# Optimization experiments

Hardware: AMD Instinct MI355X
Metric: run time of the kernel (lower is better)

Reference implementation:

```python
import jax, jax.numpy as jnp
import numpy as np

TEMPERATURE = 0.7
REDUCTION = "mean"
MARGIN = 0.5  # the '+0.5' shift inside exp in the original


def setup_inputs() -> dict:
    key = jax.random.key(0)
    k1, k2 = jax.random.split(key)
    projection = jax.random.normal(k1, (8192, 256), dtype=jnp.float32)
    y = jax.random.randint(k2, (8192,), 0, 10, dtype=jnp.int64)
    return {"projection": projection, "y": y}


def reference(projection, y):
    # L2-normalize rows, cosine similarity matrix [n, n]
    n = projection.shape[0]
    proj = projection / jnp.linalg.norm(projection, axis=1, keepdims=True)
    sim = proj @ proj.T

    eq = (y[:, None] == y[None, :]).astype(sim.dtype)
    same = eq - jnp.eye(n, dtype=sim.dtype)   # same class, excluding self
    diff = 1.0 - eq                            # different class

    # Original per-row loop computes log(1 + sum_{j in diff, k in same}
    #   exp((sim[i,j] - sim[i,k] + 0.5)/t)) which separates as
    #   exp(0.5/t) * (sum_j exp(sim[i,j]/t)) * (sum_k exp(-sim[i,k]/t)).
    # Empty set -> the loop substitutes [0], i.e. that factor becomes exp(0)=1.
    A = jnp.sum(diff * jnp.exp(sim / TEMPERATURE), axis=1)
    B = jnp.sum(same * jnp.exp(-sim / TEMPERATURE), axis=1)
    A = jnp.where(jnp.sum(diff, axis=1) > 0, A, 1.0)
    B = jnp.where(jnp.sum(same, axis=1) > 0, B, 1.0)

    loss_per_row = jnp.log1p(jnp.exp(MARGIN / TEMPERATURE) * A * B)
    if REDUCTION == "mean":
        return jnp.mean(loss_per_row)
    return jnp.sum(loss_per_row)
```

## Files before the change

### kernel.cpp

```cpp
#include <hip/hip_runtime.h>
#include <hip/hip_bf16.h>


#define NF 256
#define TINV (1.0f / 0.7f)
#define SC2 2.0609929398439434f

typedef __attribute__((ext_vector_type(8))) short short8;
typedef __attribute__((ext_vector_type(4))) float float4v;

typedef const __attribute__((address_space(1))) unsigned int glb_u32;
typedef __attribute__((address_space(3))) unsigned int lds_u32;

__global__ __launch_bounds__(256)
void k_prep(const float* __restrict__ P, unsigned short* __restrict__ Pn,
            float* __restrict__ AB) {
    int wave = threadIdx.x >> 6, lane = threadIdx.x & 63;
    int row = blockIdx.x * 4 + wave;
    if (threadIdx.x < 8) AB[blockIdx.x * 8 + threadIdx.x] = 0.f;
    float4 v = *(const float4*)(P + (size_t)row * NF + lane * 4);
    float sq = v.x * v.x + v.y * v.y + v.z * v.z + v.w * v.w;
#pragma unroll
    for (int off = 32; off; off >>= 1) sq += __shfl_xor(sq, off, 64);
    float r = rsqrtf(sq);
    __hip_bfloat16 h0 = __float2bfloat16(v.x * r), h1 = __float2bfloat16(v.y * r),
                   h2 = __float2bfloat16(v.z * r), h3 = __float2bfloat16(v.w * r);
    ushort4 o = { *(unsigned short*)&h0, *(unsigned short*)&h1,
                  *(unsigned short*)&h2, *(unsigned short*)&h3 };
    *(ushort4*)(Pn + (size_t)row * NF + lane * 4) = o;
}

__global__ __launch_bounds__(256, 2)
void k_main(const unsigned short* __restrict__ Pn, const int* __restrict__ y,
            float* __restrict__ Aacc, float* __restrict__ Bacc,
            float* __restrict__ colPart) {
    __shared__ __align__(16) unsigned short Bs[64 * NF];
    __shared__ int yc[256];
    __shared__ float colA[1024], colB[1024];

    const int tid = threadIdx.x;
    int bid = blockIdx.x;
    int C = (int)((sqrtf(4.0f * (float)bid + 1.0f) - 1.0f) * 0.5f);
    while (C * (C + 1) > bid) --C;
    while ((C + 1) * (C + 2) <= bid) ++C;
    const int I = bid - C * (C + 1);
    const int rb = I * 128, cb0 = C * 256;
    const bool colacc = (C > (I >> 1));

    const int lane = tid & 63, wave = tid >> 6;
    const int quad = lane >> 4, l15 = lane & 15;

#define DMA_CHUNK(c)                                                          \
    {                                                                         \
        _Pragma("unroll")                                                     \
        for (int i = 0; i < 8; ++i) {                                         \
            const int kc = wave * 8 + i;                                      \
            const unsigned short* src =                                       \
                Pn + (size_t)(cb0 + (c) * 64 + lane) * NF + kc * 8;           \
            __builtin_amdgcn_global_load_lds((glb_u32*)src,                   \
                (lds_u32*)&Bs[kc * 512], 16, 0, 0);                           \
        }                                                                     \
    }

    DMA_CHUNK(0)

    yc[tid] = y[cb0 + tid];
#pragma unroll
    for (int w = 0; w < 4; ++w) {
        colA[w * 256 + tid] = 0.f;
        colB[w * 256 + tid] = 0.f;
    }

    const unsigned short* pa = Pn + (size_t)(rb + wave * 32 + l15) * NF + quad * 8;
    short8 afr[2][8];
#pragma unroll
    for (int tr = 0; tr < 2; ++tr)
#pragma unroll
        for (int ks = 0; ks < 8; ++ks)
            afr[tr][ks] = *(const short8*)(pa + (size_t)tr * 16 * NF + ks * 32);

    unsigned yis[2];
#pragma unroll
    for (int tr = 0; tr < 2; ++tr) {
        int4 v = *(const int4*)(y + rb + wave * 32 + tr * 16 + quad * 4);
        yis[tr] = (unsigned)(v.x & 255) | ((unsigned)(v.y & 255) << 8) |
                  ((unsigned)(v.z & 255) << 16) | ((unsigned)(v.w & 255) << 24);
    }

    float rA[2][4], rB[2][4];
#pragma unroll
    for (int tr = 0; tr < 2; ++tr)
#pragma unroll
        for (int r = 0; r < 4; ++r) { rA[tr][r] = 0.f; rB[tr][r] = 0.f; }

#pragma unroll 1
    for (int c = 0; c < 4; ++c) {
        __syncthreads();

        float4v acc[2][4];
#pragma unroll
        for (int a = 0; a < 2; ++a)
#pragma unroll
            for (int b = 0; b < 4; ++b) acc[a][b] = (float4v){0.f, 0.f, 0.f, 0.f};

#pragma unroll
        for (int ks = 0; ks < 8; ++ks) {
            short8 fb[4];
#pragma unroll
            for (int tc = 0; tc < 4; ++tc)
                fb[tc] = *(const short8*)&Bs[(ks * 4 + quad) * 512 + (tc * 16 + l15) * 8];
#pragma unroll
            for (int tr = 0; tr < 2; ++tr)
#pragma unroll
                for (int tc = 0; tc < 4; ++tc)
                    acc[tr][tc] = __builtin_amdgcn_mfma_f32_16x16x32_bf16(
                        afr[tr][ks], fb[tc], acc[tr][tc], 0, 0, 0);
        }
        __syncthreads();
        if (c < 3) DMA_CHUNK(c + 1)

#pragma unroll
        for (int tc = 0; tc < 4; ++tc) {
            const int jl = c * 64 + tc * 16 + l15;
            const int yj = yc[jl];
            const int gj = cb0 + jl;
#pragma unroll
            for (int tr = 0; tr < 2; ++tr) {
                const int gi0 = rb + wave * 32 + tr * 16 + quad * 4;
#pragma unroll
                for (int r = 0; r < 4; ++r) {
                    const float s = acc[tr][tc][r];
                    const int cls = (yis[tr] >> (8 * r)) & 255;
                    const bool same = (cls == yj);
                    const float e = exp2f(s * (same ? -SC2 : SC2));
                    rA[tr][r] += same ? 0.f : e;
                    rB[tr][r] += (same && (gi0 + r != gj)) ? e : 0.f;
                }
            }
        }

        if (colacc) {
#pragma unroll
            for (int tc = 0; tc < 4; ++tc) {
                const int jl = c * 64 + tc * 16 + l15;
                const int yj = yc[jl];
                float ca = 0.f, cb = 0.f;
#pragma unroll
                for (int tr = 0; tr < 2; ++tr)
#pragma unroll
                    for (int r = 0; r < 4; ++r) {
                        const float s = acc[tr][tc][r];
                        const int cls = (yis[tr] >> (8 * r)) & 255;
                        const bool same = (cls == yj);
                        const float e = exp2f(s * (same ? -SC2 : SC2));
                        ca += same ? 0.f : e;
                        cb += same ? e : 0.f;
                    }
                ca += __shfl_xor(ca, 16, 64); ca += __shfl_xor(ca, 32, 64);
                cb += __shfl_xor(cb, 16, 64); cb += __shfl_xor(cb, 32, 64);
                if (quad == 0) {
                    colA[wave * 256 + jl] += ca;
                    colB[wave * 256 + jl] += cb;
                }
            }
        }
    }

#pragma unroll
    for (int tr = 0; tr < 2; ++tr)
#pragma unroll
        for (int r = 0; r < 4; ++r) {
#pragma unroll
            for (int off = 1; off < 16; off <<= 1) {
                rA[tr][r] += __shfl_xor(rA[tr][r], off, 64);
                rB[tr][r] += __shfl_xor(rB[tr][r], off, 64);
            }
        }
    if (l15 == 0) {
#pragma unroll
        for (int tr = 0; tr < 2; ++tr)
#pragma unroll
            for (int r = 0; r < 4; ++r) {
                const int gi = rb + wave * 32 + tr * 16 + quad * 4 + r;
                atomicAdd(&Aacc[gi], rA[tr][r]);
                atomicAdd(&Bacc[gi], rB[tr][r]);
            }
    }

    if (colacc) {
        __syncthreads();
        float* cp = colPart + (size_t)bid * 512;
        cp[tid]       = colA[tid] + colA[256 + tid] + colA[512 + tid] + colA[768 + tid];
        cp[256 + tid] = colB[tid] + colB[256 + tid] + colB[512 + tid] + colB[768 + tid];
    }
}

__global__ __launch_bounds__(256)
void k_reduce(const float* __restrict__ colPart, float* __restrict__ Aacc,
              float* __restrict__ Bacc) {
    const int t = threadIdx.x;
    const int jloc = t >> 1, half = t & 1;
    const int j = blockIdx.x * 128 + jloc;
    const int C = j >> 8, o = j & 255;
    const float* p = colPart + (size_t)(C * (C + 1) + half) * 512 + o;
    float sA = 0.f, sB = 0.f;
    for (int I = half; I < 2 * C; I += 2) {
        sA += p[0];
        sB += p[256];
        p += 1024;
    }
    sA += __shfl_xor(sA, 1, 64);
    sB += __shfl_xor(sB, 1, 64);
    if (half == 0) {
        Aacc[j] += sA;
        Bacc[j] += sB;
    }
}

__global__ __launch_bounds__(1024)
void k_final(const float* __restrict__ Aacc, const float* __restrict__ Bacc,
             const int* __restrict__ y, float* __restrict__ out, int n) {
    __shared__ int hist[16];
    __shared__ float red[16];
    const int tid = threadIdx.x;
    if (tid < 16) hist[tid] = 0;
    __syncthreads();
    int loc[10];
#pragma unroll
    for (int cc = 0; cc < 10; ++cc) loc[cc] = 0;
    for (int i = tid; i < n; i += 1024) {
        const int yv = y[i];
#pragma unroll
        for (int cc = 0; cc < 10; ++cc) {
            unsigned long long m = __ballot(yv == cc);
            if ((tid & 63) == 0) loc[cc] += __popcll(m);
        }
    }
    if ((tid & 63) == 0)
#pragma unroll
        for (int cc = 0; cc < 10; ++cc) atomicAdd(&hist[cc], loc[cc]);
    __syncthreads();
    const float M = __expf(0.5f * TINV);
    float s = 0.f;
    for (int i = tid; i < n; i += 1024) {
        const int cc = hist[y[i] & 15];
        const float a = (n - cc) > 0 ? Aacc[i] : 1.0f;
        const float b = (cc - 1) > 0 ? Bacc[i] : 1.0f;
        s += log1pf(M * a * b);
    }
#pragma unroll
    for (int off = 32; off; off >>= 1) s += __shfl_xor(s, off, 64);
    if ((tid & 63) == 0) red[tid >> 6] = s;
    __syncthreads();
    if (tid == 0) {
        float t = 0.f;
#pragma unroll
        for (int w = 0; w < 16; ++w) t += red[w];
        out[0] = t / (float)n;
    }
}

extern "C" void kernel_launch(void* const* d_in, const int* in_sizes, int n_in,
                              void* d_out, int out_size, void* d_ws, size_t ws_size,
                              hipStream_t stream) {
    const float* P = (const float*)d_in[0];
    const int* y   = (const int*)d_in[1];
    float* out     = (float*)d_out;
    const int n = in_sizes[1];

    unsigned short* Pn = (unsigned short*)d_ws;
    float* Aacc = (float*)((char*)d_ws + (size_t)n * NF * 2);
    float* Bacc = Aacc + n;
    float* colPart = Bacc + n;

    const int ng = n / 256;
    k_prep<<<n / 4, 256, 0, stream>>>(P, Pn, Aacc);
    k_main<<<ng * (ng + 1), 256, 0, stream>>>(Pn, y, Aacc, Bacc, colPart);
    k_reduce<<<n / 128, 256, 0, stream>>>(colPart, Aacc, Bacc);
    k_final<<<1, 1024, 0, stream>>>(Aacc, Bacc, y, out, n);
}
```

Measured before the change: 141.6 us.

## Use 128x128 triangular tiles, skip duplicate exps, fuse reduce and final kernels

The main kernel moves from 128x256 column-block tiles to 128x128 tiles over the upper triangle. Off-diagonal tiles now compute each exp once and feed both the row and column accumulators, where before the row pass and the column pass each evaluated the exp separately. Per-wave column buffers in LDS become a shared 128-entry buffer updated with LDS atomics, which shrinks LDS use. The column reduction and final log1p/mean kernels are merged into one multi-block tail kernel that writes the output with a global atomic, removing a launch and the single-block final pass, at the cost of more, smaller main blocks and LDS atomic contention.

After: 141.6 us. Within noise of the previous version (-0.0%).

```diff
diff --git a/kernel.cpp b/kernel.cpp
--- a/kernel.cpp
+++ b/kernel.cpp
@@ -14,10 +14,11 @@
 
 __global__ __launch_bounds__(256)
 void k_prep(const float* __restrict__ P, unsigned short* __restrict__ Pn,
-            float* __restrict__ AB) {
+            float* __restrict__ AB, float* __restrict__ out) {
     int wave = threadIdx.x >> 6, lane = threadIdx.x & 63;
     int row = blockIdx.x * 4 + wave;
     if (threadIdx.x < 8) AB[blockIdx.x * 8 + threadIdx.x] = 0.f;
+    if (blockIdx.x == 0 && threadIdx.x == 0) out[0] = 0.f;
     float4 v = *(const float4*)(P + (size_t)row * NF + lane * 4);
     float sq = v.x * v.x + v.y * v.y + v.z * v.z + v.w * v.w;
 #pragma unroll
@@ -35,17 +36,17 @@
             float* __restrict__ Aacc, float* __restrict__ Bacc,
             float* __restrict__ colPart) {
     __shared__ __align__(16) unsigned short Bs[64 * NF];
-    __shared__ int yc[256];
-    __shared__ float colA[1024], colB[1024];
+    __shared__ int yc[128];
+    __shared__ float colA[128], colB[128];
 
     const int tid = threadIdx.x;
     int bid = blockIdx.x;
-    int C = (int)((sqrtf(4.0f * (float)bid + 1.0f) - 1.0f) * 0.5f);
-    while (C * (C + 1) > bid) --C;
-    while ((C + 1) * (C + 2) <= bid) ++C;
-    const int I = bid - C * (C + 1);
-    const int rb = I * 128, cb0 = C * 256;
-    const bool colacc = (C > (I >> 1));
+    int C2 = (int)((sqrtf(8.0f * (float)bid + 1.0f) - 1.0f) * 0.5f);
+    while ((C2 * (C2 + 1)) / 2 > bid) --C2;
+    while (((C2 + 1) * (C2 + 2)) / 2 <= bid) ++C2;
+    const int I = bid - (C2 * (C2 + 1)) / 2;
+    const int rb = I * 128, cb0 = C2 * 128;
+    const bool offdiag = (I < C2);
 
     const int lane = tid & 63, wave = tid >> 6;
     const int quad = lane >> 4, l15 = lane & 15;
@@ -64,11 +65,10 @@
 
     DMA_CHUNK(0)
 
-    yc[tid] = y[cb0 + tid];
-#pragma unroll
-    for (int w = 0; w < 4; ++w) {
-        colA[w * 256 + tid] = 0.f;
-        colB[w * 256 + tid] = 0.f;
+    if (tid < 128) {
+        yc[tid] = y[cb0 + tid];
+        colA[tid] = 0.f;
+        colB[tid] = 0.f;
     }
 
     const unsigned short* pa = Pn + (size_t)(rb + wave * 32 + l15) * NF + quad * 8;
@@ -94,7 +94,7 @@
         for (int r = 0; r < 4; ++r) { rA[tr][r] = 0.f; rB[tr][r] = 0.f; }
 
 #pragma unroll 1
-    for (int c = 0; c < 4; ++c) {
+    for (int c = 0; c < 2; ++c) {
         __syncthreads();
 
         float4v acc[2][4];
@@ -117,29 +117,9 @@
                         afr[tr][ks], fb[tc], acc[tr][tc], 0, 0, 0);
         }
         __syncthreads();
-        if (c < 3) DMA_CHUNK(c + 1)
-
-#pragma unroll
-        for (int tc = 0; tc < 4; ++tc) {
-            const int jl = c * 64 + tc * 16 + l15;
-            const int yj = yc[jl];
-            const int gj = cb0 + jl;
-#pragma unroll
-            for (int tr = 0; tr < 2; ++tr) {
-                const int gi0 = rb + wave * 32 + tr * 16 + quad * 4;
-#pragma unroll
-                for (int r = 0; r < 4; ++r) {
-                    const float s = acc[tr][tc][r];
-                    const int cls = (yis[tr] >> (8 * r)) & 255;
-                    const bool same = (cls == yj);
-                    const float e = exp2f(s * (same ? -SC2 : SC2));
-                    rA[tr][r] += same ? 0.f : e;
-                    rB[tr][r] += (same && (gi0 + r != gj)) ? e : 0.f;
-                }
-            }
-        }
-
-        if (colacc) {
+        if (c < 1) DMA_CHUNK(1)
+
+        if (offdiag) {
 #pragma unroll
             for (int tc = 0; tc < 4; ++tc) {
                 const int jl = c * 64 + tc * 16 + l15;
@@ -153,14 +133,36 @@
                         const int cls = (yis[tr] >> (8 * r)) & 255;
                         const bool same = (cls == yj);
                         const float e = exp2f(s * (same ? -SC2 : SC2));
+                        rA[tr][r] += same ? 0.f : e;
+                        rB[tr][r] += same ? e : 0.f;
                         ca += same ? 0.f : e;
                         cb += same ? e : 0.f;
                     }
                 ca += __shfl_xor(ca, 16, 64); ca += __shfl_xor(ca, 32, 64);
                 cb += __shfl_xor(cb, 16, 64); cb += __shfl_xor(cb, 32, 64);
                 if (quad == 0) {
-                    colA[wave * 256 + jl] += ca;
-                    colB[wave * 256 + jl] += cb;
+                    atomicAdd(&colA[jl], ca);
+                    atomicAdd(&colB[jl], cb);
+                }
+            }
+        } else {
+#pragma unroll
+            for (int tc = 0; tc < 4; ++tc) {
+                const int jl = c * 64 + tc * 16 + l15;
+                const int yj = yc[jl];
+                const int gj = cb0 + jl;
+#pragma unroll
+                for (int tr = 0; tr < 2; ++tr) {
+                    const int gi0 = rb + wave * 32 + tr * 16 + quad * 4;
+#pragma unroll
+                    for (int r = 0; r < 4; ++r) {
+                        const float s = acc[tr][tc][r];
+                        const int cls = (yis[tr] >> (8 * r)) & 255;
+                        const bool same = (cls == yj);
+                        const float e = exp2f(s * (same ? -SC2 : SC2));
+                        rA[tr][r] += same ? 0.f : e;
+                        rB[tr][r] += (same && (gi0 + r != gj)) ? e : 0.f;
+                    }
                 }
             }
         }
@@ -187,48 +189,26 @@
             }
     }
 
-    if (colacc) {
+    if (offdiag) {
         __syncthreads();
-        float* cp = colPart + (size_t)bid * 512;
-        cp[tid]       = colA[tid] + colA[256 + tid] + colA[512 + tid] + colA[768 + tid];
-        cp[256 + tid] = colB[tid] + colB[256 + tid] + colB[512 + tid] + colB[768 + tid];
+        float* cp = colPart + (size_t)bid * 256;
+        cp[tid] = (tid < 128) ? colA[tid] : colB[tid - 128];
     }
 }
 
 __global__ __launch_bounds__(256)
-void k_reduce(const float* __restrict__ colPart, float* __restrict__ Aacc,
-              float* __restrict__ Bacc) {
-    const int t = threadIdx.x;
-    const int jloc = t >> 1, half = t & 1;
-    const int j = blockIdx.x * 128 + jloc;
-    const int C = j >> 8, o = j & 255;
-    const float* p = colPart + (size_t)(C * (C + 1) + half) * 512 + o;
-    float sA = 0.f, sB = 0.f;
-    for (int I = half; I < 2 * C; I += 2) {
-        sA += p[0];
-        sB += p[256];
-        p += 1024;
-    }
-    sA += __shfl_xor(sA, 1, 64);
-    sB += __shfl_xor(sB, 1, 64);
-    if (half == 0) {
-        Aacc[j] += sA;
-        Bacc[j] += sB;
-    }
-}
-
-__global__ __launch_bounds__(1024)
-void k_final(const float* __restrict__ Aacc, const float* __restrict__ Bacc,
-             const int* __restrict__ y, float* __restrict__ out, int n) {
+void k_tail(const float* __restrict__ colPart, const float* __restrict__ Aacc,
+            const float* __restrict__ Bacc, const int* __restrict__ y,
+            float* __restrict__ out, int n) {
     __shared__ int hist[16];
-    __shared__ float red[16];
+    __shared__ float red[4];
     const int tid = threadIdx.x;
     if (tid < 16) hist[tid] = 0;
     __syncthreads();
     int loc[10];
 #pragma unroll
     for (int cc = 0; cc < 10; ++cc) loc[cc] = 0;
-    for (int i = tid; i < n; i += 1024) {
+    for (int i = tid; i < n; i += 256) {
         const int yv = y[i];
 #pragma unroll
         for (int cc = 0; cc < 10; ++cc) {
@@ -240,24 +220,36 @@
 #pragma unroll
         for (int cc = 0; cc < 10; ++cc) atomicAdd(&hist[cc], loc[cc]);
     __syncthreads();
-    const float M = __expf(0.5f * TINV);
-    float s = 0.f;
-    for (int i = tid; i < n; i += 1024) {
-        const int cc = hist[y[i] & 15];
-        const float a = (n - cc) > 0 ? Aacc[i] : 1.0f;
-        const float b = (cc - 1) > 0 ? Bacc[i] : 1.0f;
-        s += log1pf(M * a * b);
-    }
-#pragma unroll
-    for (int off = 32; off; off >>= 1) s += __shfl_xor(s, off, 64);
-    if ((tid & 63) == 0) red[tid >> 6] = s;
+
+    const int jloc = tid >> 1, half = tid & 1;
+    const int j = blockIdx.x * 128 + jloc;
+    const int C2 = j >> 7, o = j & 127;
+    const float* p = colPart + ((size_t)(C2 * (C2 + 1)) / 2 + half) * 256 + o;
+    float sA = 0.f, sB = 0.f;
+    for (int I = half; I < C2; I += 2) {
+        sA += p[0];
+        sB += p[128];
+        p += 512;
+    }
+    sA += __shfl_xor(sA, 1, 64);
+    sB += __shfl_xor(sB, 1, 64);
+
+    float term = 0.f;
+    if (half == 0) {
+        const float M = __expf(0.5f * TINV);
+        const int cc = hist[y[j] & 15];
+        float a = Aacc[j] + sA;
+        float b = Bacc[j] + sB;
+        a = (n - cc) > 0 ? a : 1.0f;
+        b = (cc - 1) > 0 ? b : 1.0f;
+        term = log1pf(M * a * b);
+    }
+#pragma unroll
+    for (int off = 32; off; off >>= 1) term += __shfl_xor(term, off, 64);
+    if ((tid & 63) == 0) red[tid >> 6] = term;
     __syncthreads();
-    if (tid == 0) {
-        float t = 0.f;
-#pragma unroll
-        for (int w = 0; w < 16; ++w) t += red[w];
-        out[0] = t / (float)n;
-    }
+    if (tid == 0)
+        atomicAdd(out, (red[0] + red[1] + red[2] + red[3]) / (float)n);
 }
 
 extern "C" void kernel_launch(void* const* d_in, const int* in_sizes, int n_in,
@@ -273,9 +265,9 @@
     float* Bacc = Aacc + n;
     float* colPart = Bacc + n;
 
-    const int ng = n / 256;
-    k_prep<<<n / 4, 256, 0, stream>>>(P, Pn, Aacc);
-    k_main<<<ng * (ng + 1), 256, 0, stream>>>(Pn, y, Aacc, Bacc, colPart);
-    k_reduce<<<n / 128, 256, 0, stream>>>(colPart, Aacc, Bacc);
-    k_final<<<1, 1024, 0, stream>>>(Aacc, Bacc, y, out, n);
-}
+    const int np = n / 128;
+    const int nblk = np * (np + 1) / 2;
+    k_prep<<<n / 4, 256, 0, stream>>>(P, Pn, Aacc, out);
+    k_main<<<nblk, 256, 0, stream>>>(Pn, y, Aacc, Bacc, colPart);
+    k_tail<<<n / 128, 256, 0, stream>>>(colPart, Aacc, Bacc, y, out, n);
+}
```
